# Optimization experiments

Hardware: AMD Instinct MI355X
Metric: run time of the kernel (lower is better)

The kernel has to match this reference:

```python
import jax, jax.numpy as jnp
import numpy as np

LAMBDA_ENTROPY = 0.1
LAMBDA_REPULSION = 0.5
LAMBDA_INTER = 0.3
TEMPERATURE = 1.0
EPS = 1e-8


def setup_inputs() -> dict:
    key = jax.random.key(0)
    k1, k2 = jax.random.split(key)
    membership = jax.random.uniform(k1, (16384, 64, 32), dtype=jnp.float32)   # (N,F,K) soft bin assignments
    teacher_preds = jax.random.uniform(k2, (16384, 128), dtype=jnp.float32)   # (N,C)
    return {"membership": membership, "teacher_preds": teacher_preds}


def reference(membership, teacher_preds):
    N, F, K = membership.shape
    # --- weighted centroids per (feature, bin) ---
    bin_mass = membership.sum(axis=0) + EPS                       # (F,K)
    sum_weighted_y = jnp.einsum('nfk,nc->fkc', membership, teacher_preds)  # avoids (N,F,K,C)
    centroids = sum_weighted_y / bin_mass[..., None]              # (F,K,C)
    # --- weighted intra-bin variance: ||y_n - c_fk||^2 expanded, no (N,F,K,C) tensor ---
    y_sq = jnp.sum(teacher_preds * teacher_preds, axis=-1)        # (N,)
    c_sq = jnp.sum(centroids * centroids, axis=-1)                # (F,K)
    cross = jnp.einsum('nc,fkc->nfk', teacher_preds, centroids)   # (N,F,K)
    dist_sq = y_sq[:, None, None] + c_sq[None, :, :] - 2.0 * cross
    weighted_variance = jnp.sum(membership * dist_sq, axis=0) / bin_mass  # (F,K)
    loss_dispersion = weighted_variance.sum()
    # --- bin-occupancy entropy ---
    p_bins = bin_mass / N                                         # (F,K)
    loss_entropy = jnp.sum(p_bins * jnp.log(p_bins + EPS))
    # --- neighbor repulsion between adjacent bin centroids ---
    neighbor_dist = jnp.sum((centroids[:, :-1, :] - centroids[:, 1:, :]) ** 2, axis=-1)  # (F,K-1)
    loss_repulsion = jnp.sum(jnp.exp(-neighbor_dist / TEMPERATURE))
    # --- all-pairs inter-bin dispersion, batched over F (replaces python loop) ---
    dots = jnp.einsum('fkc,fjc->fkj', centroids, centroids)       # (F,K,K)
    pairwise = c_sq[:, :, None] + c_sq[:, None, :] - 2.0 * dots
    triu = jnp.triu(jnp.ones((K, K), dtype=centroids.dtype), k=1)  # strictly upper
    loss_inter = jnp.sum(jnp.exp(-pairwise / TEMPERATURE) * triu) / F
    total = (loss_dispersion
             + LAMBDA_ENTROPY * loss_entropy
             + LAMBDA_REPULSION * loss_repulsion
             + LAMBDA_INTER * loss_inter)
    return total, loss_dispersion, loss_entropy, loss_repulsion, loss_inter
```

## Files before the change

kernel.cpp:

```cpp
#include <hip/hip_runtime.h>
#include <math.h>

#define N_PTS   16384
#define F_DIM   64
#define K_BINS  32
#define C_DIM   128
#define FK      2048
#define CP      144
#define CW      132
#define EPS_F   1e-8f

typedef _Float16 f16x8 __attribute__((ext_vector_type(8)));
typedef float    f32x4 __attribute__((ext_vector_type(4)));

static __device__ inline unsigned pack_h2(float a, float b) {
    union { _Float16 h[2]; unsigned u; } x;
    x.h[0] = (_Float16)a; x.h[1] = (_Float16)b;
    return x.u;
}

__global__ __launch_bounds__(256) void build_yt_k(const float* __restrict__ Y,
                                                  _Float16* __restrict__ Yt) {
    __shared__ __align__(16) float Yl[64][132];
    __shared__ float ysql[64];
    const int t  = threadIdx.x;
    const int n0 = blockIdx.x * 64;
    const int nl = t >> 5;
    const int c4 = t & 31;
#pragma unroll
    for (int p = 0; p < 8; ++p) {
        const int n = p * 8 + nl;
        const float4 v = reinterpret_cast<const float4*>(Y + (size_t)(n0 + n) * C_DIM)[c4];
        reinterpret_cast<float4*>(Yl[n])[c4] = v;
        float sq = v.x * v.x + v.y * v.y + v.z * v.z + v.w * v.w;
#pragma unroll
        for (int m = 16; m >= 1; m >>= 1) sq += __shfl_xor(sq, m, 64);
        if (c4 == 0) ysql[n] = sq;
    }
    __syncthreads();
    unsigned* YtU = (unsigned*)Yt;
    const int nd0 = n0 >> 1;
    const int n2  = t & 31;
    const int rr  = t >> 5;
#pragma unroll
    for (int p = 0; p < 16; ++p) {
        const int c = p * 8 + rr;
        YtU[(size_t)c * (N_PTS / 2) + nd0 + n2] = pack_h2(Yl[2 * n2][c], Yl[2 * n2 + 1][c]);
    }
    if (t < 32) {
        YtU[(size_t)128 * (N_PTS / 2) + nd0 + t] = pack_h2(ysql[2 * t], ysql[2 * t + 1]);
    } else if (t < 64) {
        YtU[(size_t)129 * (N_PTS / 2) + nd0 + (t - 32)] = 0x3C003C00u;
    }
    for (int idx = t; idx < 14 * 32; idx += 256) {
        YtU[(size_t)(130 + (idx >> 5)) * (N_PTS / 2) + nd0 + (idx & 31)] = 0u;
    }
}

__global__ __launch_bounds__(256) void gemm_k(const float* __restrict__ M,
                                              const _Float16* __restrict__ Yt,
                                              float* __restrict__ wpart,
                                              int cn) {
    __shared__ float M_lds[32][65];
    const int t    = threadIdx.x;
    const int fk0  = blockIdx.x * 64;
    const int ch   = blockIdx.y;
    const int n0   = ch * cn;
    const int w    = t >> 6;
    const int l    = t & 63;
    const int quad = l >> 4;
    const int cl   = l & 15;
    const int fkl  = w * 16 + cl;
    const int r2   = t >> 4;
    const int fk4  = (t & 15) * 4;

    f32x4 acc[9] = {};

    const float* Mp = M + (size_t)n0 * FK + fk0 + fk4;
    float4 v0 = *reinterpret_cast<const float4*>(Mp + (size_t)(2 * r2) * FK);
    float4 v1 = *reinterpret_cast<const float4*>(Mp + (size_t)(2 * r2 + 1) * FK);

    for (int nb = 0; nb < cn; nb += 32) {
        __syncthreads();
        M_lds[2 * r2][fk4 + 0] = v0.x; M_lds[2 * r2][fk4 + 1] = v0.y;
        M_lds[2 * r2][fk4 + 2] = v0.z; M_lds[2 * r2][fk4 + 3] = v0.w;
        M_lds[2 * r2 + 1][fk4 + 0] = v1.x; M_lds[2 * r2 + 1][fk4 + 1] = v1.y;
        M_lds[2 * r2 + 1][fk4 + 2] = v1.z; M_lds[2 * r2 + 1][fk4 + 3] = v1.w;
        __syncthreads();
        if (nb + 32 < cn) {
            const float* Mn = M + (size_t)(n0 + nb + 32) * FK + fk0 + fk4;
            v0 = *reinterpret_cast<const float4*>(Mn + (size_t)(2 * r2) * FK);
            v1 = *reinterpret_cast<const float4*>(Mn + (size_t)(2 * r2 + 1) * FK);
        }
        const size_t nbq = (size_t)(n0 + nb + quad * 8);
        f16x8 b[9];
#pragma unroll
        for (int ct = 0; ct < 9; ++ct)
            b[ct] = *reinterpret_cast<const f16x8*>(Yt + (size_t)(ct * 16 + cl) * N_PTS + nbq);
        f16x8 a;
#pragma unroll
        for (int j = 0; j < 8; ++j)
            a[j] = (_Float16)M_lds[quad * 8 + j][fkl];
#pragma unroll
        for (int ct = 0; ct < 9; ++ct)
            acc[ct] = __builtin_amdgcn_mfma_f32_16x16x32_f16(a, b[ct], acc[ct], 0, 0, 0);
    }

    float* wp = wpart + (size_t)ch * FK * CW;
#pragma unroll
    for (int ct = 0; ct < 9; ++ct) {
        const int c = ct * 16 + cl;
        if (c < CW) {
#pragma unroll
            for (int rr = 0; rr < 4; ++rr) {
                const int fk = fk0 + w * 16 + quad * 4 + rr;
                wp[(size_t)fk * CW + c] = acc[ct][rr];
            }
        }
    }
}

__global__ __launch_bounds__(256) void reduce_w_k(const float* __restrict__ wpart,
                                                  float* __restrict__ W, int nchunk) {
    const int idx = blockIdx.x * 256 + threadIdx.x;
    const float4* src = reinterpret_cast<const float4*>(wpart);
    const size_t cs = (size_t)FK * CW / 4;
    float4 s = src[idx];
    for (int ch = 1; ch < nchunk; ++ch) {
        const float4 v = src[idx + (size_t)ch * cs];
        s.x += v.x; s.y += v.y; s.z += v.z; s.w += v.w;
    }
    reinterpret_cast<float4*>(W)[idx] = s;
}

__global__ __launch_bounds__(256) void epilogue_k(const float* __restrict__ W,
                                                  float* __restrict__ fpart) {
    __shared__ __align__(16) float Wl[32][CW];
    __shared__ float Bv[32], Binv[32], S1v[32], csq[32];
    __shared__ float scr[32][8];
    __shared__ float4 red4[256];
    const int t = threadIdx.x;
    const int f = blockIdx.x;

    for (int e = t; e < 32 * 33; e += 256) {
        const int k = e / 33, c4 = e % 33;
        reinterpret_cast<float4*>(Wl[k])[c4] =
            reinterpret_cast<const float4*>(W + (size_t)(f * 32 + k) * CW)[c4];
    }
    __syncthreads();
    if (t < 32) {
        const float B = Wl[t][129] + EPS_F;
        Bv[t] = B; Binv[t] = 1.0f / B; S1v[t] = Wl[t][128];
    }
    __syncthreads();
    {
        const int k = t >> 3, g = t & 7;
        const float ib = Binv[k];
        float s = 0.f;
        for (int c = g * 16; c < g * 16 + 16; ++c) {
            const float v = Wl[k][c] * ib;
            Wl[k][c] = v;
            s = fmaf(v, v, s);
        }
        scr[k][g] = s;
    }
    __syncthreads();
    if (t < 32) {
        float s = 0.f;
#pragma unroll
        for (int g = 0; g < 8; ++g) s += scr[t][g];
        csq[t] = s;
    }
    __syncthreads();

    float my_disp = 0.f, my_ent = 0.f, my_rep = 0.f, my_inter = 0.f;
    if (t < 32) {
        my_disp = (S1v[t] - csq[t] * (Bv[t] + EPS_F)) * Binv[t];
        const float p = Bv[t] * (1.0f / (float)N_PTS);
        my_ent = p * logf(p + EPS_F);
    }
    {
        const int pr = t >> 3, g = t & 7;
        float s = 0.f;
        if (pr < 31) {
            for (int c = g * 16; c < g * 16 + 16; ++c) {
                const float d = Wl[pr][c] - Wl[pr + 1][c];
                s = fmaf(d, d, s);
            }
        }
        __syncthreads();
        scr[pr][g] = s;
    }
    __syncthreads();
    if (t < 31) {
        float d = 0.f;
#pragma unroll
        for (int g = 0; g < 8; ++g) d += scr[t][g];
        my_rep = expf(-d);
    }
#pragma unroll
    for (int s4 = 0; s4 < 4; ++s4) {
        const int slot = t + s4 * 256;
        const int k = slot >> 5, j = slot & 31;
        if (k < j) {
            float dot = 0.f;
            for (int c4 = 0; c4 < 32; ++c4) {
                const float4 a = reinterpret_cast<const float4*>(Wl[k])[c4];
                const float4 b = reinterpret_cast<const float4*>(Wl[j])[c4];
                dot = fmaf(a.x, b.x, dot); dot = fmaf(a.y, b.y, dot);
                dot = fmaf(a.z, b.z, dot); dot = fmaf(a.w, b.w, dot);
            }
            my_inter += expf(-(csq[k] + csq[j] - 2.0f * dot));
        }
    }
    red4[t] = make_float4(my_disp, my_ent, my_rep, my_inter);
    __syncthreads();
    for (int off = 128; off >= 1; off >>= 1) {
        if (t < off) {
            const float4 a = red4[t], b = red4[t + off];
            red4[t] = make_float4(a.x + b.x, a.y + b.y, a.z + b.z, a.w + b.w);
        }
        __syncthreads();
    }
    if (t == 0) {
        fpart[f * 4 + 0] = red4[0].x;
        fpart[f * 4 + 1] = red4[0].y;
        fpart[f * 4 + 2] = red4[0].z;
        fpart[f * 4 + 3] = red4[0].w;
    }
}

__global__ void final_reduce_k(const float* __restrict__ fpart,
                               float* __restrict__ out) {
    const int t = threadIdx.x;
    float4 v = reinterpret_cast<const float4*>(fpart)[t];
#pragma unroll
    for (int m = 32; m >= 1; m >>= 1) {
        v.x += __shfl_xor(v.x, m, 64);
        v.y += __shfl_xor(v.y, m, 64);
        v.z += __shfl_xor(v.z, m, 64);
        v.w += __shfl_xor(v.w, m, 64);
    }
    if (t == 0) {
        const float disp  = v.x, ent = v.y, rep = v.z;
        const float inter = v.w * (1.0f / (float)F_DIM);
        out[0] = disp + 0.1f * ent + 0.5f * rep + 0.3f * inter;
        out[1] = disp;
        out[2] = ent;
        out[3] = rep;
        out[4] = inter;
    }
}

extern "C" void kernel_launch(void* const* d_in, const int* in_sizes, int n_in,
                              void* d_out, int out_size, void* d_ws, size_t ws_size,
                              hipStream_t stream) {
    const float* M = (const float*)d_in[0];
    const float* Y = (const float*)d_in[1];
    float* out = (float*)d_out;
    char*  ws  = (char*)d_ws;

    const size_t ytBytes = (size_t)CP * N_PTS * sizeof(_Float16);
    const size_t wBytes  = (size_t)FK * CW * sizeof(float);

    _Float16* Yt    = (_Float16*)ws;
    float*    W     = (float*)(ws + ytBytes);
    float*    fpart = (float*)(ws + ytBytes + wBytes);
    float*    wpart = (float*)(ws + ytBytes + wBytes + 1024);

    const size_t used = ytBytes + wBytes + 1024;
    int nchunk = 32;
    while (nchunk > 1 && used + (size_t)nchunk * wBytes > ws_size) nchunk >>= 1;
    const int cn = N_PTS / nchunk;

    build_yt_k<<<dim3(N_PTS / 64), dim3(256), 0, stream>>>(Y, Yt);
    gemm_k<<<dim3(32, nchunk), dim3(256), 0, stream>>>(M, Yt, wpart, cn);
    reduce_w_k<<<dim3(FK * CW / 4 / 256), dim3(256), 0, stream>>>(wpart, W, nchunk);
    epilogue_k<<<dim3(F_DIM), dim3(256), 0, stream>>>(W, fpart);
    final_reduce_k<<<dim3(1), dim3(64), 0, stream>>>(fpart, out);
}
```

Before: 270.2 us.

## Double fk tile per block, load M directly to registers, unroll chunk reduction

The GEMM kernel now covers 128 fk columns per block with two MFMA row tiles per wave, so each loaded Yt fragment feeds two MFMAs. The LDS staging, double-buffered prefetch and barriers for M are gone; each lane instead does scalar strided global loads of M rows straight into f16 fragments, which may hurt coalescing. The partial-sum reduction runs with 4 independent accumulators over chunks and 128-thread blocks. Halving the grid raises per-block work but lowers occupancy and parallelism.

```diff
diff --git a/kernel.cpp b/kernel.cpp
--- a/kernel.cpp
+++ b/kernel.cpp
@@ -61,76 +61,83 @@
                                               const _Float16* __restrict__ Yt,
                                               float* __restrict__ wpart,
                                               int cn) {
-    __shared__ float M_lds[32][65];
     const int t    = threadIdx.x;
-    const int fk0  = blockIdx.x * 64;
+    const int fk0  = blockIdx.x * 128;
     const int ch   = blockIdx.y;
     const int n0   = ch * cn;
     const int w    = t >> 6;
     const int l    = t & 63;
     const int quad = l >> 4;
     const int cl   = l & 15;
-    const int fkl  = w * 16 + cl;
-    const int r2   = t >> 4;
-    const int fk4  = (t & 15) * 4;
-
-    f32x4 acc[9] = {};
-
-    const float* Mp = M + (size_t)n0 * FK + fk0 + fk4;
-    float4 v0 = *reinterpret_cast<const float4*>(Mp + (size_t)(2 * r2) * FK);
-    float4 v1 = *reinterpret_cast<const float4*>(Mp + (size_t)(2 * r2 + 1) * FK);
+    const int fkA  = fk0 + w * 32 + cl;
+
+    f32x4 acc[2][9] = {};
 
     for (int nb = 0; nb < cn; nb += 32) {
-        __syncthreads();
-        M_lds[2 * r2][fk4 + 0] = v0.x; M_lds[2 * r2][fk4 + 1] = v0.y;
-        M_lds[2 * r2][fk4 + 2] = v0.z; M_lds[2 * r2][fk4 + 3] = v0.w;
-        M_lds[2 * r2 + 1][fk4 + 0] = v1.x; M_lds[2 * r2 + 1][fk4 + 1] = v1.y;
-        M_lds[2 * r2 + 1][fk4 + 2] = v1.z; M_lds[2 * r2 + 1][fk4 + 3] = v1.w;
-        __syncthreads();
-        if (nb + 32 < cn) {
-            const float* Mn = M + (size_t)(n0 + nb + 32) * FK + fk0 + fk4;
-            v0 = *reinterpret_cast<const float4*>(Mn + (size_t)(2 * r2) * FK);
-            v1 = *reinterpret_cast<const float4*>(Mn + (size_t)(2 * r2 + 1) * FK);
-        }
-        const size_t nbq = (size_t)(n0 + nb + quad * 8);
+        const int nbase = n0 + nb + quad * 8;
         f16x8 b[9];
 #pragma unroll
         for (int ct = 0; ct < 9; ++ct)
-            b[ct] = *reinterpret_cast<const f16x8*>(Yt + (size_t)(ct * 16 + cl) * N_PTS + nbq);
-        f16x8 a;
-#pragma unroll
-        for (int j = 0; j < 8; ++j)
-            a[j] = (_Float16)M_lds[quad * 8 + j][fkl];
-#pragma unroll
-        for (int ct = 0; ct < 9; ++ct)
-            acc[ct] = __builtin_amdgcn_mfma_f32_16x16x32_f16(a, b[ct], acc[ct], 0, 0, 0);
+            b[ct] = *reinterpret_cast<const f16x8*>(
+                Yt + (size_t)(ct * 16 + cl) * N_PTS + nbase);
+        f16x8 a0, a1;
+#pragma unroll
+        for (int j = 0; j < 8; ++j) {
+            const float* row = M + (size_t)(nbase + j) * FK;
+            a0[j] = (_Float16)row[fkA];
+            a1[j] = (_Float16)row[fkA + 16];
+        }
+#pragma unroll
+        for (int ct = 0; ct < 9; ++ct) {
+            acc[0][ct] = __builtin_amdgcn_mfma_f32_16x16x32_f16(a0, b[ct], acc[0][ct], 0, 0, 0);
+            acc[1][ct] = __builtin_amdgcn_mfma_f32_16x16x32_f16(a1, b[ct], acc[1][ct], 0, 0, 0);
+        }
     }
 
     float* wp = wpart + (size_t)ch * FK * CW;
 #pragma unroll
-    for (int ct = 0; ct < 9; ++ct) {
-        const int c = ct * 16 + cl;
-        if (c < CW) {
-#pragma unroll
-            for (int rr = 0; rr < 4; ++rr) {
-                const int fk = fk0 + w * 16 + quad * 4 + rr;
-                wp[(size_t)fk * CW + c] = acc[ct][rr];
+    for (int mt = 0; mt < 2; ++mt) {
+#pragma unroll
+        for (int ct = 0; ct < 9; ++ct) {
+            const int c = ct * 16 + cl;
+            if (c < CW) {
+#pragma unroll
+                for (int r = 0; r < 4; ++r) {
+                    const int fk = fk0 + w * 32 + mt * 16 + quad * 4 + r;
+                    wp[(size_t)fk * CW + c] = acc[mt][ct][r];
+                }
             }
         }
     }
 }
 
-__global__ __launch_bounds__(256) void reduce_w_k(const float* __restrict__ wpart,
+__global__ __launch_bounds__(128) void reduce_w_k(const float* __restrict__ wpart,
                                                   float* __restrict__ W, int nchunk) {
-    const int idx = blockIdx.x * 256 + threadIdx.x;
+    const int idx = blockIdx.x * 128 + threadIdx.x;
     const float4* src = reinterpret_cast<const float4*>(wpart);
     const size_t cs = (size_t)FK * CW / 4;
-    float4 s = src[idx];
-    for (int ch = 1; ch < nchunk; ++ch) {
-        const float4 v = src[idx + (size_t)ch * cs];
-        s.x += v.x; s.y += v.y; s.z += v.z; s.w += v.w;
-    }
-    reinterpret_cast<float4*>(W)[idx] = s;
+    float4 s0 = make_float4(0.f, 0.f, 0.f, 0.f), s1 = s0, s2 = s0, s3 = s0;
+    int ch = 0;
+    for (; ch + 3 < nchunk; ch += 4) {
+        const float4 a = src[idx + (size_t)(ch + 0) * cs];
+        const float4 b = src[idx + (size_t)(ch + 1) * cs];
+        const float4 c = src[idx + (size_t)(ch + 2) * cs];
+        const float4 d = src[idx + (size_t)(ch + 3) * cs];
+        s0.x += a.x; s0.y += a.y; s0.z += a.z; s0.w += a.w;
+        s1.x += b.x; s1.y += b.y; s1.z += b.z; s1.w += b.w;
+        s2.x += c.x; s2.y += c.y; s2.z += c.z; s2.w += c.w;
+        s3.x += d.x; s3.y += d.y; s3.z += d.z; s3.w += d.w;
+    }
+    for (; ch < nchunk; ++ch) {
+        const float4 a = src[idx + (size_t)ch * cs];
+        s0.x += a.x; s0.y += a.y; s0.z += a.z; s0.w += a.w;
+    }
+    float4 r;
+    r.x = (s0.x + s1.x) + (s2.x + s3.x);
+    r.y = (s0.y + s1.y) + (s2.y + s3.y);
+    r.z = (s0.z + s1.z) + (s2.z + s3.z);
+    r.w = (s0.w + s1.w) + (s2.w + s3.w);
+    reinterpret_cast<float4*>(W)[idx] = r;
 }
 
 __global__ __launch_bounds__(256) void epilogue_k(const float* __restrict__ W,
@@ -274,8 +281,8 @@
     const int cn = N_PTS / nchunk;
 
     build_yt_k<<<dim3(N_PTS / 64), dim3(256), 0, stream>>>(Y, Yt);
-    gemm_k<<<dim3(32, nchunk), dim3(256), 0, stream>>>(M, Yt, wpart, cn);
-    reduce_w_k<<<dim3(FK * CW / 4 / 256), dim3(256), 0, stream>>>(wpart, W, nchunk);
+    gemm_k<<<dim3(16, nchunk), dim3(256), 0, stream>>>(M, Yt, wpart, cn);
+    reduce_w_k<<<dim3(FK * CW / 4 / 128), dim3(128), 0, stream>>>(wpart, W, nchunk);
     epilogue_k<<<dim3(F_DIM), dim3(256), 0, stream>>>(W, fpart);
     final_reduce_k<<<dim3(1), dim3(64), 0, stream>>>(fpart, out);
 }
```

Measured after the change: 241.3 us. 10.7% less time.
